# Optimization experiments

Measured on AMD Instinct MI355X. Metric: run time of the kernel, lower is better.

## Reference

```python
import jax, jax.numpy as jnp
import numpy as np
from jax import lax

DIM, HEADS, BS, TOPK, WIN = 256, 8, 8, 4, 7
HID = 2 * DIM  # DBFFN ffn_expansion_factor=2
B, H, W = 2, 56, 56


def _lin(x, w, b=None):
    # torch Linear: y = x @ W.T + b, W is [out, in]
    y = jnp.einsum('...c,oc->...o', x, w)
    return y if b is None else y + b


def _ln(x, w, b, eps=1e-6):
    mu = jnp.mean(x, -1, keepdims=True)
    var = jnp.mean((x - mu) ** 2, -1, keepdims=True)
    return (x - mu) * lax.rsqrt(var + eps) * w + b


def _mha(Q, K, V, wq_w, wq_b, wk_w, wk_b, wv_w, wv_b, p_w, p_b):
    # standard cross MHA: Q [B,Nq,C], K/V [B,Nk,C]
    Bq, Nq, C = Q.shape
    h, d = HEADS, C // HEADS
    scale = d ** -0.5
    q = _lin(Q, wq_w, wq_b).reshape(Bq, Nq, h, d)
    k = _lin(K, wk_w, wk_b).reshape(Bq, -1, h, d)
    v = _lin(V, wv_w, wv_b).reshape(Bq, -1, h, d)
    attn = jax.nn.softmax(jnp.einsum('bnhd,bmhd->bhnm', q, k) * scale, axis=-1)
    out = jnp.einsum('bhnm,bmhd->bnhd', attn, v).reshape(Bq, Nq, C)
    return _lin(out, p_w, p_b)


def setup_inputs() -> dict:
    key = jax.random.key(0)
    ks = jax.random.split(key, 16)
    s = 0.02
    C = DIM
    inp = {
        'x': jax.random.normal(ks[0], (B, C, H, W), jnp.float32),
        'pos_w': jax.random.normal(ks[1], (C, 1, 3, 3), jnp.float32) * s,
        'pos_b': jnp.zeros((C,), jnp.float32),
        'n1_w': jnp.ones((C,), jnp.float32), 'n1_b': jnp.zeros((C,), jnp.float32),
        'n2_w': jnp.ones((C,), jnp.float32), 'n2_b': jnp.zeros((C,), jnp.float32),
        'wq_w': jax.random.normal(ks[2], (3, C, C), jnp.float32) * s,
        'wq_b': jnp.zeros((3, C), jnp.float32),
        'wk_w': jax.random.normal(ks[3], (3, C, C), jnp.float32) * s,
        'wk_b': jnp.zeros((3, C), jnp.float32),
        'wv_w': jax.random.normal(ks[4], (3, C, C), jnp.float32) * s,
        'wv_b': jnp.zeros((3, C), jnp.float32),
        'pj_w': jax.random.normal(ks[5], (3, C, C), jnp.float32) * s,
        'pj_b': jnp.zeros((3, C), jnp.float32),
        # block scorer
        's1_w': jax.random.normal(ks[6], (C // 2, C), jnp.float32) * s,
        's1_b': jnp.zeros((C // 2,), jnp.float32),
        's2_w': jax.random.normal(ks[7], (1, C // 2), jnp.float32) * s,
        's2_b': jnp.zeros((1,), jnp.float32),
        # gating: per-token softmax weights over 3 branches
        'g_w': jax.random.normal(ks[8], (3, C), jnp.float32) * s,
        'g_b': jnp.zeros((3,), jnp.float32),
        # DBFFN (gated dconv FFN, bias=False): in-proj C->2*HID, dw 3x3, out-proj HID->C
        'pin_w': jax.random.normal(ks[9], (2 * HID, C), jnp.float32) * s,
        'dw_w': jax.random.normal(ks[10], (3, 3, 1, 2 * HID), jnp.float32) * s,
        'pout_w': jax.random.normal(ks[11], (C, HID), jnp.float32) * s,
    }
    return inp


def _forward(x, pos_w, pos_b, n1_w, n1_b, n2_w, n2_b, wq_w, wq_b, wk_w, wk_b,
             wv_w, wv_b, pj_w, pj_b, s1_w, s1_b, s2_w, s2_b, g_w, g_b,
             pin_w, dw_w, pout_w):
    Bx, C, Hx, Wx = x.shape
    # depthwise positional conv
    pos = lax.conv_general_dilated(x, pos_w, (1, 1), 'SAME',
                                   dimension_numbers=('NCHW', 'OIHW', 'NCHW'),
                                   feature_group_count=C)
    x = x + pos + pos_b[None, :, None, None] * 0 + pos_b[None, :, None, None]
    feat = jnp.transpose(x, (0, 2, 3, 1))  # NHWC
    Nq = Hx * Wx
    Q = feat.reshape(Bx, Nq, C)
    # block means
    nH, nW = Hx // BS, Wx // BS
    nB = nH * nW
    blk = feat.reshape(Bx, nH, BS, nW, BS, C).transpose(0, 1, 3, 2, 4, 5)
    blk = blk.reshape(Bx, nB, BS * BS, C).mean(axis=2)  # [B,nB,C]
    # block scores + top-k selection
    hsc = jax.nn.gelu(_lin(blk, s1_w, s1_b), approximate=False)
    scores = _lin(hsc, s2_w, s2_b)[..., 0]  # [B,nB]
    topk = min(TOPK, nB)
    _, idx = lax.top_k(scores, topk)
    K_sel = jnp.take_along_axis(blk, idx[:, :, None], axis=1)  # [B,topk,C]
    # compressed + selected branches
    y_cmp = _mha(Q, blk, blk, wq_w[0], wq_b[0], wk_w[0], wk_b[0], wv_w[0], wv_b[0], pj_w[0], pj_b[0])
    y_sel = _mha(Q, K_sel, K_sel, wq_w[1], wq_b[1], wk_w[1], wk_b[1], wv_w[1], wv_b[1], pj_w[1], pj_b[1])
    # local window branch (replicate-pad + unfold == shifted slices)
    pad = WIN // 2
    padded = jnp.pad(feat, ((0, 0), (pad, pad), (pad, pad), (0, 0)), mode='edge')
    patches = jnp.stack([padded[:, dy:dy + Hx, dx:dx + Wx, :]
                         for dy in range(WIN) for dx in range(WIN)], axis=3)
    patches = patches.reshape(Bx, Nq, WIN * WIN, C)  # [B,Nq,49,C]
    h, d = HEADS, C // HEADS
    scale = d ** -0.5
    q = _lin(Q, wq_w[2], wq_b[2]).reshape(Bx, Nq, h, d)
    k = _lin(patches, wk_w[2], wk_b[2]).reshape(Bx, Nq, WIN * WIN, h, d)
    v = _lin(patches, wv_w[2], wv_b[2]).reshape(Bx, Nq, WIN * WIN, h, d)
    attn = jax.nn.softmax(jnp.einsum('bnhd,bnwhd->bnhw', q, k) * scale, axis=-1)
    y_win = jnp.einsum('bnhw,bnwhd->bnhd', attn, v).reshape(Bx, Nq, C)
    y_win = _lin(y_win, pj_w[2], pj_b[2])
    # gated fusion + residual
    qn = _ln(Q, n1_w, n1_b)
    g = jax.nn.softmax(_lin(qn, g_w, g_b), axis=-1)  # [B,Nq,3]
    y = g[..., 0:1] * y_cmp + g[..., 1:2] * y_sel + g[..., 2:3] * y_win + Q
    ym = y.reshape(Bx, Hx, Wx, C)
    # DBFFN: gated depthwise-conv FFN (bias-free)
    t = _lin(ym, pin_w)  # [B,H,W,2*HID]
    t = lax.conv_general_dilated(t, dw_w, (1, 1), 'SAME',
                                 dimension_numbers=('NHWC', 'HWIO', 'NHWC'),
                                 feature_group_count=2 * HID)
    x1, x2 = jnp.split(t, 2, axis=-1)
    mlp = _lin(jax.nn.gelu(x1, approximate=False) * x2, pout_w)
    ym = _ln(ym + mlp, n2_w, n2_b)
    return jnp.transpose(ym, (0, 3, 1, 2))  # NCHW


def reference(x, pos_w, pos_b, n1_w, n1_b, n2_w, n2_b, wq_w, wq_b, wk_w, wk_b,
              wv_w, wv_b, pj_w, pj_b, s1_w, s1_b, s2_w, s2_b, g_w, g_b,
              pin_w, dw_w, pout_w):
    return _forward(x, pos_w, pos_b, n1_w, n1_b, n2_w, n2_b, wq_w, wq_b, wk_w,
                    wk_b, wv_w, wv_b, pj_w, pj_b, s1_w, s1_b, s2_w, s2_b,
                    g_w, g_b, pin_w, dw_w, pout_w)
```

## Files before the change

kernel.cpp:

```cpp
#include <hip/hip_runtime.h>

#define BATCH 2
#define CDIM 256
#define HEADS 8
#define HD 32
#define HH 56
#define WW 56
#define NQ 3136
#define NTOK 6272
#define NB 49
#define NTOPK 4
#define HID2 1024
#define HIDM 512
#define QSTR 768
#define KVSTR 512
#define ASTR 768

typedef short bf16x8 __attribute__((ext_vector_type(8)));
typedef float f32x4 __attribute__((ext_vector_type(4)));
typedef _Float16 h2 __attribute__((ext_vector_type(2)));
struct __align__(16) h2x4 { h2 x, y, z, w; };

__device__ __forceinline__ float blockReduce256(float v, float* red) {
    #pragma unroll
    for (int off = 32; off > 0; off >>= 1) v += __shfl_xor(v, off);
    if ((threadIdx.x & 63) == 0) red[threadIdx.x >> 6] = v;
    __syncthreads();
    float r = red[0] + red[1] + red[2] + red[3];
    __syncthreads();
    return r;
}

__device__ __forceinline__ float gelu_exact(float x) {
    return 0.5f * x * (1.f + erff(x * 0.70710678118654752f));
}

__device__ __forceinline__ short f2bf(float f) {
    union { float f; unsigned u; } v; v.f = f;
    unsigned r = v.u + 0x7FFFu + ((v.u >> 16) & 1u);
    return (short)(r >> 16);
}

__device__ __forceinline__ float fdot2h(h2 a, h2 b, float c) {
#if __has_builtin(__builtin_amdgcn_fdot2)
    return __builtin_amdgcn_fdot2(a, b, c, false);
#else
    return c + (float)a[0] * (float)b[0] + (float)a[1] * (float)b[1];
#endif
}

__device__ __forceinline__ void gld16(const void* gsrc, void* ldst) {
    __builtin_amdgcn_global_load_lds(
        (const __attribute__((address_space(1))) void*)gsrc,
        (__attribute__((address_space(3))) void*)ldst, 16, 0, 0);
}

__global__ __launch_bounds__(256) void k_wcvt(
        const float* __restrict__ wq_w, const float* __restrict__ wk_w,
        const float* __restrict__ wv_w, const float* __restrict__ wq_b,
        const float* __restrict__ wk_b, const float* __restrict__ wv_b,
        const float* __restrict__ pj_w, const float* __restrict__ pin_w,
        const float* __restrict__ pout_w,
        short* __restrict__ Wc1, short* __restrict__ Wpj,
        short* __restrict__ Wpin, short* __restrict__ Wpout,
        float* __restrict__ bias1, float* __restrict__ Wkv0,
        float* __restrict__ bkv0, float* __restrict__ Wkv1,
        float* __restrict__ bkv1) {
    int i = blockIdx.x * 256 + threadIdx.x;
    if (i < 327680) {
        int r = i >> 8, k = i & 255, seg = r >> 8, n = r & 255;
        float v;
        if (seg == 0)      v = wq_w[n * 256 + k];
        else if (seg == 1) v = wq_w[65536 + n * 256 + k];
        else if (seg == 2) v = wq_w[131072 + n * 256 + k];
        else if (seg == 3) v = wk_w[131072 + n * 256 + k];
        else               v = wv_w[131072 + n * 256 + k];
        Wc1[i] = f2bf(v);
    } else if (i < 524288) {
        int j = i - 327680;
        int n = j / 768, t = j % 768, br = t >> 8, k = t & 255;
        Wpj[j] = f2bf(pj_w[br * 65536 + n * 256 + k]);
    } else if (i < 786432) {
        int j = i - 524288;
        Wpin[j] = f2bf(pin_w[j]);
    } else if (i < 917504) {
        int j = i - 786432;
        Wpout[j] = f2bf(pout_w[j]);
    } else if (i < 1048576) {
        int j = i - 917504;
        int r = j >> 8, k = j & 255;
        Wkv0[j] = (r < 256) ? wk_w[r * 256 + k] : wv_w[(r - 256) * 256 + k];
    } else if (i < 1179648) {
        int j = i - 1048576;
        int r = j >> 8, k = j & 255;
        Wkv1[j] = (r < 256) ? wk_w[65536 + r * 256 + k] : wv_w[65536 + (r - 256) * 256 + k];
    } else if (i < 1180928) {
        int j = i - 1179648;
        float v;
        if (j < 768)       v = wq_b[j];
        else if (j < 1024) v = wk_b[512 + (j - 768)];
        else               v = wv_b[512 + (j - 1024)];
        bias1[j] = v;
    } else if (i < 1181440) {
        int j = i - 1180928;
        bkv0[j] = (j < 256) ? wk_b[j] : wv_b[j - 256];
    } else if (i < 1181952) {
        int j = i - 1181440;
        bkv1[j] = (j < 256) ? wk_b[256 + j] : wv_b[j];
    }
}

__global__ __launch_bounds__(256) void k_tr(const float* __restrict__ x,
                                            float* __restrict__ xT) {
    __shared__ float t[64][65];
    int p0 = blockIdx.x * 64;
    int c0 = blockIdx.y * 64;
    int b  = blockIdx.z;
    int tid = threadIdx.x;
    int pi = tid & 63, cj = tid >> 6;
    #pragma unroll
    for (int j = 0; j < 16; j++) {
        int c = cj * 16 + j;
        t[c][pi] = x[((size_t)(b * CDIM + c0 + c)) * NQ + p0 + pi];
    }
    __syncthreads();
    int ci = tid & 63, pj = tid >> 6;
    #pragma unroll
    for (int j = 0; j < 16; j++) {
        int p = pj * 16 + j;
        xT[((size_t)(b * NQ + p0 + p)) * CDIM + c0 + ci] = t[ci][p];
    }
}

__global__ __launch_bounds__(256) void k_posgates(
        const float* __restrict__ xT, const float* __restrict__ pw,
        const float* __restrict__ pb, const float* __restrict__ n1w,
        const float* __restrict__ n1b, const float* __restrict__ gw,
        const float* __restrict__ gb, float* __restrict__ feat,
        float* __restrict__ g, short* __restrict__ featb) {
    __shared__ float red[4];
    int bn = blockIdx.x;
    int b = bn / NQ, n = bn % NQ;
    int y = n / WW, x = n % WW;
    int c = threadIdx.x;
    float wv[9];
    #pragma unroll
    for (int i = 0; i < 9; i++) wv[i] = pw[c * 9 + i];
    const float* xb = xT + (size_t)b * NQ * CDIM;
    float acc = xb[(size_t)n * CDIM + c] + pb[c];
    #pragma unroll
    for (int dy = 0; dy < 3; dy++) {
        int yy = y + dy - 1;
        if (yy < 0 || yy >= HH) continue;
        #pragma unroll
        for (int dx = 0; dx < 3; dx++) {
            int xx = x + dx - 1;
            if (xx < 0 || xx >= WW) continue;
            acc += xb[((size_t)(yy * WW + xx)) * CDIM + c] * wv[dy * 3 + dx];
        }
    }
    feat[(size_t)bn * CDIM + c] = acc;
    featb[(size_t)bn * CDIM + c] = f2bf(acc);
    float mu = blockReduce256(acc, red) * (1.f / CDIM);
    float d = acc - mu;
    float var = blockReduce256(d * d, red) * (1.f / CDIM);
    float qn = d * rsqrtf(var + 1e-6f) * n1w[c] + n1b[c];
    float l0 = blockReduce256(qn * gw[c], red) + gb[0];
    float l1 = blockReduce256(qn * gw[CDIM + c], red) + gb[1];
    float l2 = blockReduce256(qn * gw[2 * CDIM + c], red) + gb[2];
    if (c < 3) {
        float m3 = fmaxf(l0, fmaxf(l1, l2));
        float e0 = __expf(l0 - m3), e1 = __expf(l1 - m3), e2 = __expf(l2 - m3);
        float inv = 1.f / (e0 + e1 + e2);
        float e = (c == 0) ? e0 : (c == 1) ? e1 : e2;
        g[bn * 3 + c] = e * inv;
    }
}

__global__ __launch_bounds__(256) void k_blkscore(
        const float* __restrict__ feat, const float* __restrict__ s1w,
        const float* __restrict__ s1b, const float* __restrict__ s2w,
        const float* __restrict__ s2b, float* __restrict__ blk,
        float* __restrict__ scores) {
    __shared__ float sblk[256];
    __shared__ float red[128];
    int gid = blockIdx.x;
    int b = gid / NB, bid = gid % NB;
    int by = bid / 7, bx = bid % 7;
    int c = threadIdx.x;
    float s = 0.f;
    for (int iy = 0; iy < 8; iy++)
        for (int ix = 0; ix < 8; ix++) {
            int y = by * 8 + iy, xx = bx * 8 + ix;
            s += feat[((size_t)(b * NQ + y * WW + xx)) * CDIM + c];
        }
    s *= (1.f / 64.f);
    blk[(size_t)gid * CDIM + c] = s;
    sblk[c] = s;
    __syncthreads();
    if (c < 128) {
        const float* wrow = s1w + (size_t)c * CDIM;
        float acc = s1b[c];
        for (int k = 0; k < CDIM; k++) acc += sblk[k] * wrow[k];
        red[c] = gelu_exact(acc) * s2w[c];
    }
    __syncthreads();
    #pragma unroll
    for (int st = 64; st > 0; st >>= 1) {
        if (c < st) red[c] += red[c + st];
        __syncthreads();
    }
    if (c == 0) scores[gid] = red[0] + s2b[0];
}

__global__ __launch_bounds__(256) void k_gemm64kv(
        const float* __restrict__ blk, const float* __restrict__ Wkv0,
        const float* __restrict__ bkv0, _Float16* __restrict__ kvcmp,
        const float* __restrict__ scores, const float* __restrict__ Wkv1,
        const float* __restrict__ bkv1, _Float16* __restrict__ kvsel) {
    __shared__ float As[16][68];
    __shared__ float Ws[16][68];
    __shared__ float ssc[2][NB];
    __shared__ int sidx[8];
    const float* W; const float* bias; _Float16* C; int M;
    int m0;
    bool sel = (blockIdx.y == 2);
    if (!sel) { W = Wkv0; bias = bkv0; C = kvcmp; M = 98; m0 = blockIdx.y * 64; }
    else      { W = Wkv1; bias = bkv1; C = kvsel; M = 8;  m0 = 0; }
    const int N = 512, K = 256;
    const int tid = threadIdx.x;
    const int tx = tid & 15, ty = tid >> 4;
    const int n0 = blockIdx.x * 64;
    const int lr = tid >> 2;
    const int lk = (tid & 3) * 4;
    if (sel) {
        if (tid < 2 * NB) ssc[tid / NB][tid % NB] = scores[tid];
        __syncthreads();
        if (tid < 2) {
            for (int t = 0; t < NTOPK; t++) {
                int best = 0; float bv = -1e30f;
                for (int m = 0; m < NB; m++)
                    if (ssc[tid][m] > bv) { bv = ssc[tid][m]; best = m; }
                sidx[tid * 4 + t] = best; ssc[tid][best] = -1e30f;
            }
        }
        __syncthreads();
    }
    int gm = m0 + lr;
    int arow = gm;
    if (sel && gm < 8) arow = (gm >> 2) * NB + sidx[gm];
    float acc[4][4] = {};
    for (int k0 = 0; k0 < K; k0 += 16) {
        float4 av = make_float4(0.f, 0.f, 0.f, 0.f);
        if (gm < M) av = *(const float4*)(blk + (size_t)arow * K + k0 + lk);
        int gn = n0 + lr;
        float4 wv = make_float4(0.f, 0.f, 0.f, 0.f);
        if (gn < N) wv = *(const float4*)(W + (size_t)gn * K + k0 + lk);
        __syncthreads();
        As[lk][lr] = av.x; As[lk + 1][lr] = av.y; As[lk + 2][lr] = av.z; As[lk + 3][lr] = av.w;
        Ws[lk][lr] = wv.x; Ws[lk + 1][lr] = wv.y; Ws[lk + 2][lr] = wv.z; Ws[lk + 3][lr] = wv.w;
        __syncthreads();
        #pragma unroll
        for (int kk = 0; kk < 16; kk++) {
            const float4 a = *(const float4*)&As[kk][ty * 4];
            const float4 b = *(const float4*)&Ws[kk][tx * 4];
            acc[0][0] += a.x * b.x; acc[0][1] += a.x * b.y; acc[0][2] += a.x * b.z; acc[0][3] += a.x * b.w;
            acc[1][0] += a.y * b.x; acc[1][1] += a.y * b.y; acc[1][2] += a.y * b.z; acc[1][3] += a.y * b.w;
            acc[2][0] += a.z * b.x; acc[2][1] += a.z * b.y; acc[2][2] += a.z * b.z; acc[2][3] += a.z * b.w;
            acc[3][0] += a.w * b.x; acc[3][1] += a.w * b.y; acc[3][2] += a.w * b.z; acc[3][3] += a.w * b.w;
        }
    }
    #pragma unroll
    for (int i = 0; i < 4; i++) {
        int om = m0 + ty * 4 + i;
        if (om >= M) break;
        #pragma unroll
        for (int j = 0; j < 4; j++) {
            int gn = n0 + tx * 4 + j;
            C[(size_t)om * N + gn] = (_Float16)(acc[i][j] + bias[gn]);
        }
    }
}

__global__ __launch_bounds__(256) void k_gemm_mfma128(
        const short* __restrict__ A, const short* __restrict__ W,
        const float* __restrict__ bias, float* __restrict__ C,
        int M, int N, int K, int Nc, int cstr, _Float16* __restrict__ C2) {
    __shared__ short As[128][40];
    __shared__ short Bs[128][40];
    int tid = threadIdx.x;
    int wid = tid >> 6, lane = tid & 63;
    int wm = wid >> 1, wn = wid & 1;
    int m0 = blockIdx.y * 128, n0 = blockIdx.x * 128;
    f32x4 acc[4][4] = {};
    int ar = tid >> 1, ac = (tid & 1) * 16;
    int fr = lane & 15, fk = (lane >> 4) * 8;
    for (int k0 = 0; k0 < K; k0 += 32) {
        const short* ap = A + (size_t)(m0 + ar) * K + k0 + ac;
        bf16x8 a0 = *(const bf16x8*)(ap);
        bf16x8 a1 = *(const bf16x8*)(ap + 8);
        const short* wp = W + (size_t)(n0 + ar) * K + k0 + ac;
        bf16x8 wv0 = *(const bf16x8*)(wp);
        bf16x8 wv1 = *(const bf16x8*)(wp + 8);
        __syncthreads();
        *(bf16x8*)&As[ar][ac] = a0;
        *(bf16x8*)&As[ar][ac + 8] = a1;
        *(bf16x8*)&Bs[ar][ac] = wv0;
        *(bf16x8*)&Bs[ar][ac + 8] = wv1;
        __syncthreads();
        bf16x8 af[4], bf[4];
        #pragma unroll
        for (int mi = 0; mi < 4; mi++)
            af[mi] = *(const bf16x8*)&As[wm * 64 + mi * 16 + fr][fk];
        #pragma unroll
        for (int ni = 0; ni < 4; ni++)
            bf[ni] = *(const bf16x8*)&Bs[wn * 64 + ni * 16 + fr][fk];
        #pragma unroll
        for (int mi = 0; mi < 4; mi++)
            #pragma unroll
            for (int ni = 0; ni < 4; ni++)
                acc[mi][ni] = __builtin_amdgcn_mfma_f32_16x16x32_bf16(
                    af[mi], bf[ni], acc[mi][ni], 0, 0, 0);
    }
    int rsub = (lane >> 4) * 4;
    #pragma unroll
    for (int mi = 0; mi < 4; mi++) {
        #pragma unroll
        for (int ni = 0; ni < 4; ni++) {
            int col = n0 + wn * 64 + ni * 16 + (lane & 15);
            float bv = bias ? bias[col] : 0.f;
            #pragma unroll
            for (int r = 0; r < 4; r++) {
                int row = m0 + wm * 64 + mi * 16 + rsub + r;
                float v = acc[mi][ni][r] + bv;
                if (col < Nc) C[(size_t)row * cstr + col] = v;
                else          C2[(size_t)row * (N - Nc) + (col - Nc)] = (_Float16)v;
            }
        }
    }
}

__global__ __launch_bounds__(256) void k_gemm_mfma(
        const short* __restrict__ A, const short* __restrict__ W,
        const float* __restrict__ bias, float* __restrict__ C,
        int M, int N, int K,
        const float* __restrict__ resid, const float* __restrict__ g3,
        const float* __restrict__ pjb, short* __restrict__ Cb) {
    __shared__ short As[128][40];
    __shared__ short Bs[64][40];
    int tid = threadIdx.x;
    int wid = tid >> 6, lane = tid & 63;
    int wm = wid >> 1, wn = wid & 1;
    int m0 = blockIdx.y * 128, n0 = blockIdx.x * 64;
    f32x4 acc[4][2] = {};
    int ar = tid >> 1, ac = (tid & 1) * 16;
    int br = tid >> 2, bc = (tid & 3) * 8;
    int fr = lane & 15, fk = (lane >> 4) * 8;
    for (int k0 = 0; k0 < K; k0 += 32) {
        const short* ap = A + (size_t)(m0 + ar) * K + k0 + ac;
        bf16x8 a0 = *(const bf16x8*)(ap);
        bf16x8 a1 = *(const bf16x8*)(ap + 8);
        bf16x8 wv = *(const bf16x8*)(W + (size_t)(n0 + br) * K + k0 + bc);
        __syncthreads();
        *(bf16x8*)&As[ar][ac] = a0;
        *(bf16x8*)&As[ar][ac + 8] = a1;
        *(bf16x8*)&Bs[br][bc] = wv;
        __syncthreads();
        bf16x8 af[4], bf[2];
        #pragma unroll
        for (int mi = 0; mi < 4; mi++)
            af[mi] = *(const bf16x8*)&As[wm * 64 + mi * 16 + fr][fk];
        #pragma unroll
        for (int ni = 0; ni < 2; ni++)
            bf[ni] = *(const bf16x8*)&Bs[wn * 32 + ni * 16 + fr][fk];
        #pragma unroll
        for (int mi = 0; mi < 4; mi++)
            #pragma unroll
            for (int ni = 0; ni < 2; ni++)
                acc[mi][ni] = __builtin_amdgcn_mfma_f32_16x16x32_bf16(
                    af[mi], bf[ni], acc[mi][ni], 0, 0, 0);
    }
    int rsub = (lane >> 4) * 4;
    #pragma unroll
    for (int mi = 0; mi < 4; mi++) {
        #pragma unroll
        for (int ni = 0; ni < 2; ni++) {
            int col = n0 + wn * 32 + ni * 16 + (lane & 15);
            #pragma unroll
            for (int r = 0; r < 4; r++) {
                int row = m0 + wm * 64 + mi * 16 + rsub + r;
                float v = acc[mi][ni][r];
                if (resid) {
                    v += resid[(size_t)row * N + col]
                       + g3[row * 3 + 0] * pjb[col]
                       + g3[row * 3 + 1] * pjb[256 + col]
                       + g3[row * 3 + 2] * pjb[512 + col];
                } else if (bias) {
                    v += bias[col];
                }
                C[(size_t)row * N + col] = v;
                if (Cb) Cb[(size_t)row * N + col] = f2bf(v);
            }
        }
    }
}

__global__ __launch_bounds__(256) void k_attn_lds(
        const float* __restrict__ bufQ, const _Float16* __restrict__ kvc,
        const _Float16* __restrict__ kvs, short* __restrict__ Acatb,
        const float* __restrict__ g, const _Float16* __restrict__ KVw) {
    __shared__ uint4 buf[80 * 32];
    int tid = threadIdx.x;
    int wid = tid >> 6;
    int lane = tid & 63;
    int l = tid & 31;
    int tk = tid >> 5;
    int dg = l & 3;
    int co = l * 8;
    const float scale = 0.17677669529663687f;

    if (blockIdx.x < 784) {
        int bid = blockIdx.x;
        int swz = (bid & 7) * 98 + (bid >> 3);
        int t0 = swz * 8;
        int tok = t0 + tk;
        int b = t0 / NQ;
        const _Float16* kb = kvc + (size_t)b * NB * 512;
        for (int p = wid * 2; p < NB + 1; p += 8) {
            int myp = p + (lane >> 5);
            if (myp > NB - 1) myp = NB - 1;
            gld16((const uint4*)(kb + (size_t)myp * 512) + (lane & 31), &buf[p * 32]);
        }
        const float* qrow = bufQ + (size_t)tok * QSTR;
        float gate0 = g[tok * 3 + 0];
        float gate1 = g[tok * 3 + 1];
        short* orow = Acatb + (size_t)tok * ASTR;
        h2 qh0, qh1, qh2, qh3;
        {
            const float* qp = qrow + co;
            float4 q0 = *(const float4*)(qp);
            float4 q1 = *(const float4*)(qp + 4);
            qh0[0] = (_Float16)q0.x; qh0[1] = (_Float16)q0.y;
            qh1[0] = (_Float16)q0.z; qh1[1] = (_Float16)q0.w;
            qh2[0] = (_Float16)q1.x; qh2[1] = (_Float16)q1.y;
            qh3[0] = (_Float16)q1.z; qh3[1] = (_Float16)q1.w;
        }
        __syncthreads();
        float sc[13];
        sc[12] = -1e30f;
        #pragma unroll
        for (int m = 0; m < NB; m++) {
            h2x4 kv = *(const h2x4*)&buf[m * 32 + l];
            float acc = fdot2h(qh0, kv.x, 0.f);
            acc = fdot2h(qh1, kv.y, acc);
            acc = fdot2h(qh2, kv.z, acc);
            acc = fdot2h(qh3, kv.w, acc);
            acc += __shfl_xor(acc, 1);
            acc += __shfl_xor(acc, 2);
            if ((m & 3) == dg) sc[m >> 2] = acc * scale;
        }
        float mx = sc[0];
        #pragma unroll
        for (int i = 1; i < 13; i++) mx = fmaxf(mx, sc[i]);
        mx = fmaxf(mx, __shfl_xor(mx, 1));
        mx = fmaxf(mx, __shfl_xor(mx, 2));
        float sum = 0.f;
        #pragma unroll
        for (int i = 0; i < 13; i++) { sc[i] = __expf(sc[i] - mx); sum += sc[i]; }
        sum += __shfl_xor(sum, 1);
        sum += __shfl_xor(sum, 2);
        float inv_c = 1.f / sum;
        __syncthreads();
        for (int p = wid * 2; p < NB + 1; p += 8) {
            int myp = p + (lane >> 5);
            if (myp > NB - 1) myp = NB - 1;
            gld16((const uint4*)(kb + (size_t)myp * 512 + 256) + (lane & 31), &buf[p * 32]);
        }
        {
            const _Float16* ksb = kvs + (size_t)b * NTOPK * 512;
            h2 sh0, sh1, sh2, sh3;
            {
                const float* qp = qrow + 256 + co;
                float4 q0 = *(const float4*)(qp);
                float4 q1 = *(const float4*)(qp + 4);
                sh0[0] = (_Float16)q0.x; sh0[1] = (_Float16)q0.y;
                sh1[0] = (_Float16)q0.z; sh1[1] = (_Float16)q0.w;
                sh2[0] = (_Float16)q1.x; sh2[1] = (_Float16)q1.y;
                sh3[0] = (_Float16)q1.z; sh3[1] = (_Float16)q1.w;
            }
            float sv = 0.f;
            #pragma unroll
            for (int m = 0; m < NTOPK; m++) {
                h2x4 kk = *(const h2x4*)(ksb + (size_t)m * 512 + co);
                float acc = fdot2h(sh0, kk.x, 0.f);
                acc = fdot2h(sh1, kk.y, acc);
                acc = fdot2h(sh2, kk.z, acc);
                acc = fdot2h(sh3, kk.w, acc);
                acc += __shfl_xor(acc, 1);
                acc += __shfl_xor(acc, 2);
                if (m == dg) sv = acc * scale;
            }
            float mxs = sv;
            mxs = fmaxf(mxs, __shfl_xor(mxs, 1));
            mxs = fmaxf(mxs, __shfl_xor(mxs, 2));
            float e = __expf(sv - mxs);
            float sums = e;
            sums += __shfl_xor(sums, 1);
            sums += __shfl_xor(sums, 2);
            float invs = 1.f / sums;
            float o[8];
            #pragma unroll
            for (int d = 0; d < 8; d++) o[d] = 0.f;
            #pragma unroll
            for (int m = 0; m < NTOPK; m++) {
                float pw = __shfl(e, m, 4);
                h2x4 vv = *(const h2x4*)(ksb + (size_t)m * 512 + 256 + co);
                o[0] += pw * (float)vv.x[0]; o[1] += pw * (float)vv.x[1];
                o[2] += pw * (float)vv.y[0]; o[3] += pw * (float)vv.y[1];
                o[4] += pw * (float)vv.z[0]; o[5] += pw * (float)vv.z[1];
                o[6] += pw * (float)vv.w[0]; o[7] += pw * (float)vv.w[1];
            }
            float gg = gate1 * invs;
            bf16x8 ov;
            #pragma unroll
            for (int d = 0; d < 8; d++) ov[d] = f2bf(o[d] * gg);
            *(bf16x8*)(orow + 256 + co) = ov;
        }
        __syncthreads();
        {
            float o[8];
            #pragma unroll
            for (int d = 0; d < 8; d++) o[d] = 0.f;
            #pragma unroll
            for (int m = 0; m < NB; m++) {
                float pw = __shfl(sc[m >> 2], m & 3, 4);
                h2x4 vv = *(const h2x4*)&buf[m * 32 + l];
                o[0] += pw * (float)vv.x[0]; o[1] += pw * (float)vv.x[1];
                o[2] += pw * (float)vv.y[0]; o[3] += pw * (float)vv.y[1];
                o[4] += pw * (float)vv.z[0]; o[5] += pw * (float)vv.z[1];
                o[6] += pw * (float)vv.w[0]; o[7] += pw * (float)vv.w[1];
            }
            float gg = gate0 * inv_c;
            bf16x8 ov;
            #pragma unroll
            for (int d = 0; d < 8; d++) ov[d] = f2bf(o[d] * gg);
            *(bf16x8*)(orow + co) = ov;
        }
    } else {
        int bid = blockIdx.x - 784;
        int swz = (bid & 7) * 98 + (bid >> 3);
        int b = swz / 392;
        int r = swz % 392;
        int y0 = (r / 14) * 2;
        int x0 = (r % 14) * 4;
        int ty = tk >> 2, tx = tk & 3;
        int y = y0 + ty, x = x0 + tx;
        int tok = b * NQ + y * WW + x;
        const _Float16* KVb = KVw + (size_t)b * NQ * KVSTR;
        for (int p = wid * 2; p < 80; p += 8) {
            int pp = p + (lane >> 5);
            int pr = pp / 10, pc = pp - pr * 10;
            int gy = min(max(y0 + pr - 3, 0), HH - 1);
            int gx = min(max(x0 + pc - 3, 0), WW - 1);
            gld16((const uint4*)(KVb + (size_t)(gy * WW + gx) * KVSTR) + (lane & 31),
                  &buf[p * 32]);
        }
        h2 qh0, qh1, qh2, qh3;
        {
            const float* qp = bufQ + ((size_t)tok) * QSTR + 512 + co;
            float4 q0 = *(const float4*)(qp);
            float4 q1 = *(const float4*)(qp + 4);
            qh0[0] = (_Float16)q0.x; qh0[1] = (_Float16)q0.y;
            qh1[0] = (_Float16)q0.z; qh1[1] = (_Float16)q0.w;
            qh2[0] = (_Float16)q1.x; qh2[1] = (_Float16)q1.y;
            qh3[0] = (_Float16)q1.z; qh3[1] = (_Float16)q1.w;
        }
        float gate = g[tok * 3 + 2];
        __syncthreads();
        float sw[13];
        sw[12] = -1e30f;
        #pragma unroll
        for (int dy = 0; dy < 7; dy++) {
            #pragma unroll
            for (int dx = 0; dx < 7; dx++) {
                int p = (ty + dy) * 10 + tx + dx;
                h2x4 kv = *(const h2x4*)&buf[p * 32 + l];
                float acc = fdot2h(qh0, kv.x, 0.f);
                acc = fdot2h(qh1, kv.y, acc);
                acc = fdot2h(qh2, kv.z, acc);
                acc = fdot2h(qh3, kv.w, acc);
                acc += __shfl_xor(acc, 1);
                acc += __shfl_xor(acc, 2);
                int m = dy * 7 + dx;
                if ((m & 3) == dg) sw[m >> 2] = acc * scale;
            }
        }
        float mx = sw[0];
        #pragma unroll
        for (int i = 1; i < 13; i++) mx = fmaxf(mx, sw[i]);
        mx = fmaxf(mx, __shfl_xor(mx, 1));
        mx = fmaxf(mx, __shfl_xor(mx, 2));
        float sum = 0.f;
        #pragma unroll
        for (int i = 0; i < 13; i++) { sw[i] = __expf(sw[i] - mx); sum += sw[i]; }
        sum += __shfl_xor(sum, 1);
        sum += __shfl_xor(sum, 2);
        float inv = 1.f / sum;
        __syncthreads();
        for (int p = wid * 2; p < 80; p += 8) {
            int pp = p + (lane >> 5);
            int pr = pp / 10, pc = pp - pr * 10;
            int gy = min(max(y0 + pr - 3, 0), HH - 1);
            int gx = min(max(x0 + pc - 3, 0), WW - 1);
            gld16((const uint4*)(KVb + (size_t)(gy * WW + gx) * KVSTR + 256) + (lane & 31),
                  &buf[p * 32]);
        }
        __syncthreads();
        float o[8];
        #pragma unroll
        for (int d = 0; d < 8; d++) o[d] = 0.f;
        #pragma unroll
        for (int dy = 0; dy < 7; dy++) {
            #pragma unroll
            for (int dx = 0; dx < 7; dx++) {
                int p = (ty + dy) * 10 + tx + dx;
                int m = dy * 7 + dx;
                float pw = __shfl(sw[m >> 2], m & 3, 4);
                h2x4 vv = *(const h2x4*)&buf[p * 32 + l];
                o[0] += pw * (float)vv.x[0]; o[1] += pw * (float)vv.x[1];
                o[2] += pw * (float)vv.y[0]; o[3] += pw * (float)vv.y[1];
                o[4] += pw * (float)vv.z[0]; o[5] += pw * (float)vv.z[1];
                o[6] += pw * (float)vv.w[0]; o[7] += pw * (float)vv.w[1];
            }
        }
        float gg = gate * inv;
        short* op = Acatb + (size_t)tok * ASTR + 512 + co;
        bf16x8 ov;
        #pragma unroll
        for (int d = 0; d < 8; d++) ov[d] = f2bf(o[d] * gg);
        *(bf16x8*)(op) = ov;
    }
}

__global__ __launch_bounds__(256) void k_dwglu2(
        const float* __restrict__ t, const float* __restrict__ w,
        short* __restrict__ G) {
    int gid = blockIdx.x;
    int xq = gid & 3;
    int y = (gid >> 2) % HH;
    int b = gid / (HH * 4);
    int c = threadIdx.x;
    float wv[9][4];
    #pragma unroll
    for (int i = 0; i < 9; i++)
        #pragma unroll
        for (int j = 0; j < 4; j++) wv[i][j] = w[i * HID2 + c + j * 256];
    const float* tb = t + (size_t)b * NQ * HID2;
    short* Gbase = G + (size_t)b * NQ * HIDM;
    int x0 = xq * 14;
    float col[3][12];
    #pragma unroll
    for (int ci = 0; ci < 2; ci++) {
        int xx = x0 - 1 + ci;
        #pragma unroll
        for (int r = 0; r < 3; r++) {
            int yy = y + r - 1;
            bool ok = (xx >= 0) && (yy >= 0) && (yy < HH);
            const float* row = ok ? (tb + ((size_t)(yy * WW + xx)) * HID2 + c) : nullptr;
            #pragma unroll
            for (int j = 0; j < 4; j++)
                col[ci][r * 4 + j] = ok ? row[j * 256] : 0.f;
        }
    }
    #pragma unroll
    for (int i = 0; i < 14; i++) {
        int xx = x0 + i;
        {
            int xl = xx + 1;
            #pragma unroll
            for (int r = 0; r < 3; r++) {
                int yy = y + r - 1;
                bool ok = (xl < WW) && (yy >= 0) && (yy < HH);
                const float* row = ok ? (tb + ((size_t)(yy * WW + xl)) * HID2 + c) : nullptr;
                #pragma unroll
                for (int j = 0; j < 4; j++)
                    col[(i + 2) % 3][r * 4 + j] = ok ? row[j * 256] : 0.f;
            }
        }
        float a0 = 0.f, a1 = 0.f, a2 = 0.f, a3 = 0.f;
        #pragma unroll
        for (int r = 0; r < 3; r++) {
            #pragma unroll
            for (int dxx = 0; dxx < 3; dxx++) {
                const float* cc = col[(i + dxx) % 3];
                int wi = r * 3 + dxx;
                a0 += cc[r * 4 + 0] * wv[wi][0];
                a1 += cc[r * 4 + 1] * wv[wi][1];
                a2 += cc[r * 4 + 2] * wv[wi][2];
                a3 += cc[r * 4 + 3] * wv[wi][3];
            }
        }
        short* Gb = Gbase + (size_t)(y * WW + xx) * HIDM;
        Gb[c]       = f2bf(gelu_exact(a0) * a2);
        Gb[c + 256] = f2bf(gelu_exact(a1) * a3);
    }
}

__global__ __launch_bounds__(256) void k_finalln(
        const float* __restrict__ ym, const float* __restrict__ mlp,
        const float* __restrict__ n2w, const float* __restrict__ n2b,
        float* __restrict__ ymn) {
    __shared__ float red[4];
    int bn = blockIdx.x, c = threadIdx.x;
    size_t base = (size_t)bn * CDIM;
    float v = ym[base + c] + mlp[base + c];
    float mu = blockReduce256(v, red) * (1.f / CDIM);
    float d = v - mu;
    float var = blockReduce256(d * d, red) * (1.f / CDIM);
    ymn[base + c] = d * rsqrtf(var + 1e-6f) * n2w[c] + n2b[c];
}

__global__ __launch_bounds__(256) void k_tr2(const float* __restrict__ ymn,
                                             float* __restrict__ out) {
    __shared__ float t[64][65];
    int p0 = blockIdx.x * 64;
    int c0 = blockIdx.y * 64;
    int b  = blockIdx.z;
    int tid = threadIdx.x;
    int ci = tid & 63, pj = tid >> 6;
    #pragma unroll
    for (int j = 0; j < 16; j++) {
        int p = pj * 16 + j;
        t[ci][p] = ymn[((size_t)(b * NQ + p0 + p)) * CDIM + c0 + ci];
    }
    __syncthreads();
    int pi = tid & 63, cj = tid >> 6;
    #pragma unroll
    for (int j = 0; j < 16; j++) {
        int c = cj * 16 + j;
        out[((size_t)(b * CDIM + c0 + c)) * NQ + p0 + pi] = t[c][pi];
    }
}

extern "C" void kernel_launch(void* const* d_in, const int* in_sizes, int n_in,
                              void* d_out, int out_size, void* d_ws, size_t ws_size,
                              hipStream_t stream) {
    const float* x     = (const float*)d_in[0];
    const float* pos_w = (const float*)d_in[1];
    const float* pos_b = (const float*)d_in[2];
    const float* n1w   = (const float*)d_in[3];
    const float* n1b   = (const float*)d_in[4];
    const float* n2w   = (const float*)d_in[5];
    const float* n2b   = (const float*)d_in[6];
    const float* wq_w  = (const float*)d_in[7];
    const float* wq_b  = (const float*)d_in[8];
    const float* wk_w  = (const float*)d_in[9];
    const float* wk_b  = (const float*)d_in[10];
    const float* wv_w  = (const float*)d_in[11];
    const float* wv_b  = (const float*)d_in[12];
    const float* pj_w  = (const float*)d_in[13];
    const float* pj_b  = (const float*)d_in[14];
    const float* s1w   = (const float*)d_in[15];
    const float* s1b   = (const float*)d_in[16];
    const float* s2w   = (const float*)d_in[17];
    const float* s2b   = (const float*)d_in[18];
    const float* gw    = (const float*)d_in[19];
    const float* gb    = (const float*)d_in[20];
    const float* pinw  = (const float*)d_in[21];
    const float* dww   = (const float*)d_in[22];
    const float* poutw = (const float*)d_in[23];
    float* out = (float*)d_out;
    float* ws  = (float*)d_ws;

    const size_t SZ = (size_t)NTOK * CDIM;
    float* feat = ws;
    float* bufQ = feat + SZ;
    float* R1   = bufQ + (size_t)NTOK * QSTR;
    float* xT   = R1;
    short* Acatb = (short*)R1;
    float* T1   = R1;
    float* ym   = R1 + (size_t)NTOK * 1024;
    _Float16* KVw = (_Float16*)(ym + SZ);
    float* ymn  = (float*)KVw;
    short* featb = (short*)((float*)KVw + SZ);
    short* ymb   = featb + (size_t)NTOK * CDIM;
    float* blk   = (float*)(ymb + (size_t)NTOK * CDIM);
    _Float16* kvcmp = (_Float16*)(blk + 98 * 256);
    _Float16* kvsel = kvcmp + 98 * 512;
    float* scores = (float*)(kvsel + 8 * 512);
    float* g      = scores + 128;
    float* bias1  = g + (size_t)NTOK * 3;
    float* Wkv0   = bias1 + 1280;
    float* bkv0   = Wkv0 + 512 * 256;
    float* Wkv1   = bkv0 + 512;
    float* bkv1   = Wkv1 + 512 * 256;
    short* Wc1    = (short*)(bkv1 + 512);
    short* Wpj    = Wc1 + 1280 * 256;
    short* Wpin   = Wpj + 256 * 768;
    short* Wpout  = Wpin + 1024 * 256;
    short* G      = (short*)bufQ;
    float* MLP    = bufQ + (size_t)NTOK * CDIM;

    hipLaunchKernelGGL(k_wcvt, dim3(4618), dim3(256), 0, stream,
                       wq_w, wk_w, wv_w, wq_b, wk_b, wv_b, pj_w, pinw, poutw,
                       Wc1, Wpj, Wpin, Wpout, bias1, Wkv0, bkv0, Wkv1, bkv1);
    hipLaunchKernelGGL(k_tr, dim3(49, 4, BATCH), dim3(256), 0, stream, x, xT);
    hipLaunchKernelGGL(k_posgates, dim3(NTOK), dim3(256), 0, stream,
                       xT, pos_w, pos_b, n1w, n1b, gw, gb, feat, g, featb);
    hipLaunchKernelGGL(k_blkscore, dim3(BATCH * NB), dim3(256), 0, stream,
                       feat, s1w, s1b, s2w, s2b, blk, scores);
    hipLaunchKernelGGL(k_gemm64kv, dim3(8, 3), dim3(256), 0, stream,
                       blk, Wkv0, bkv0, kvcmp, scores, Wkv1, bkv1, kvsel);
    hipLaunchKernelGGL(k_gemm_mfma128, dim3(1280 / 128, NTOK / 128), dim3(256), 0, stream,
                       featb, Wc1, bias1, bufQ, NTOK, 1280, 256, 768, QSTR, KVw);
    hipLaunchKernelGGL(k_attn_lds, dim3(1568), dim3(256), 0, stream,
                       bufQ, kvcmp, kvsel, Acatb, g, KVw);
    hipLaunchKernelGGL(k_gemm_mfma, dim3(CDIM / 64, NTOK / 128), dim3(256), 0, stream,
                       Acatb, Wpj, nullptr, ym, NTOK, CDIM, ASTR, feat, g, pj_b, ymb);
    hipLaunchKernelGGL(k_gemm_mfma128, dim3(HID2 / 128, NTOK / 128), dim3(256), 0, stream,
                       ymb, Wpin, nullptr, T1, NTOK, HID2, 256, HID2, HID2, (_Float16*)nullptr);
    hipLaunchKernelGGL(k_dwglu2, dim3(BATCH * HH * 4), dim3(256), 0, stream, T1, dww, G);
    hipLaunchKernelGGL(k_gemm_mfma, dim3(CDIM / 64, NTOK / 128), dim3(256), 0, stream,
                       G, Wpout, nullptr, MLP, NTOK, CDIM, HIDM,
                       nullptr, nullptr, nullptr, (short*)nullptr);
    hipLaunchKernelGGL(k_finalln, dim3(NTOK), dim3(256), 0, stream, ym, MLP, n2w, n2b, ymn);
    hipLaunchKernelGGL(k_tr2, dim3(49, 4, BATCH), dim3(256), 0, stream, ymn, out);
}
```

Measured before the change: 194.8 us.

## Store QKV and FFN intermediates as fp16, and use one wave per token in posgates

The fused QKV GEMM now writes a single fp16 buffer with a 1280-element row stride, replacing the fp32 Q buffer plus a separate fp16 KV buffer. The attention kernel reads Q directly as packed halves, with no per-lane conversion. The FFN input-projection output T1 is also stored in fp16 and consumed by the depthwise GLU kernel, roughly halving the traffic of the largest intermediate. k_posgates is restructured so each 64-lane wave handles whole tokens with float4 loads and shuffle-only reductions, removing block-level syncs, and the workspace layout is reshuffled to fit. The trade-off is extra fp16 rounding of Q and T1, plus reliance on the unseen GEMM kernel handling the half-only output path at the new stride.

Measured after the change: 230.7 us. 1.18x slower.

```diff
diff --git a/kernel.cpp b/kernel.cpp
--- a/kernel.cpp
+++ b/kernel.cpp
@@ -12,24 +12,13 @@
 #define NTOPK 4
 #define HID2 1024
 #define HIDM 512
-#define QSTR 768
-#define KVSTR 512
+#define QSTRH 1280
 #define ASTR 768
 
 typedef short bf16x8 __attribute__((ext_vector_type(8)));
 typedef float f32x4 __attribute__((ext_vector_type(4)));
 typedef _Float16 h2 __attribute__((ext_vector_type(2)));
 struct __align__(16) h2x4 { h2 x, y, z, w; };
-
-__device__ __forceinline__ float blockReduce256(float v, float* red) {
-    #pragma unroll
-    for (int off = 32; off > 0; off >>= 1) v += __shfl_xor(v, off);
-    if ((threadIdx.x & 63) == 0) red[threadIdx.x >> 6] = v;
-    __syncthreads();
-    float r = red[0] + red[1] + red[2] + red[3];
-    __syncthreads();
-    return r;
-}
 
 __device__ __forceinline__ float gelu_exact(float x) {
     return 0.5f * x * (1.f + erff(x * 0.70710678118654752f));
@@ -138,42 +127,81 @@
         const float* __restrict__ n1b, const float* __restrict__ gw,
         const float* __restrict__ gb, float* __restrict__ feat,
         float* __restrict__ g, short* __restrict__ featb) {
-    __shared__ float red[4];
-    int bn = blockIdx.x;
-    int b = bn / NQ, n = bn % NQ;
-    int y = n / WW, x = n % WW;
-    int c = threadIdx.x;
-    float wv[9];
-    #pragma unroll
-    for (int i = 0; i < 9; i++) wv[i] = pw[c * 9 + i];
-    const float* xb = xT + (size_t)b * NQ * CDIM;
-    float acc = xb[(size_t)n * CDIM + c] + pb[c];
-    #pragma unroll
-    for (int dy = 0; dy < 3; dy++) {
-        int yy = y + dy - 1;
-        if (yy < 0 || yy >= HH) continue;
-        #pragma unroll
-        for (int dx = 0; dx < 3; dx++) {
-            int xx = x + dx - 1;
-            if (xx < 0 || xx >= WW) continue;
-            acc += xb[((size_t)(yy * WW + xx)) * CDIM + c] * wv[dy * 3 + dx];
-        }
-    }
-    feat[(size_t)bn * CDIM + c] = acc;
-    featb[(size_t)bn * CDIM + c] = f2bf(acc);
-    float mu = blockReduce256(acc, red) * (1.f / CDIM);
-    float d = acc - mu;
-    float var = blockReduce256(d * d, red) * (1.f / CDIM);
-    float qn = d * rsqrtf(var + 1e-6f) * n1w[c] + n1b[c];
-    float l0 = blockReduce256(qn * gw[c], red) + gb[0];
-    float l1 = blockReduce256(qn * gw[CDIM + c], red) + gb[1];
-    float l2 = blockReduce256(qn * gw[2 * CDIM + c], red) + gb[2];
-    if (c < 3) {
-        float m3 = fmaxf(l0, fmaxf(l1, l2));
-        float e0 = __expf(l0 - m3), e1 = __expf(l1 - m3), e2 = __expf(l2 - m3);
-        float inv = 1.f / (e0 + e1 + e2);
-        float e = (c == 0) ? e0 : (c == 1) ? e1 : e2;
-        g[bn * 3 + c] = e * inv;
+    int wvid = threadIdx.x >> 6;
+    int lane = threadIdx.x & 63;
+    int c4 = lane * 4;
+    float pwv[4][9];
+    #pragma unroll
+    for (int j = 0; j < 4; j++)
+        #pragma unroll
+        for (int i = 0; i < 9; i++) pwv[j][i] = pw[(c4 + j) * 9 + i];
+    float4 pbv = *(const float4*)(pb + c4);
+    float4 w1 = *(const float4*)(n1w + c4);
+    float4 b1 = *(const float4*)(n1b + c4);
+    float4 gw0 = *(const float4*)(gw + c4);
+    float4 gw1 = *(const float4*)(gw + CDIM + c4);
+    float4 gw2 = *(const float4*)(gw + 2 * CDIM + c4);
+    float gb0 = gb[0], gb1 = gb[1], gb2 = gb[2];
+    int tbase = blockIdx.x * 16 + wvid * 4;
+    for (int t = 0; t < 4; t++) {
+        int bn = tbase + t;
+        int b = bn / NQ, n = bn % NQ;
+        int y = n / WW, x = n % WW;
+        const float* xb = xT + (size_t)b * NQ * CDIM;
+        float4 a = *(const float4*)(xb + (size_t)n * CDIM + c4);
+        float acc0 = a.x + pbv.x, acc1 = a.y + pbv.y;
+        float acc2 = a.z + pbv.z, acc3 = a.w + pbv.w;
+        #pragma unroll
+        for (int dy = 0; dy < 3; dy++) {
+            int yy = y + dy - 1;
+            if (yy < 0 || yy >= HH) continue;
+            #pragma unroll
+            for (int dx = 0; dx < 3; dx++) {
+                int xx = x + dx - 1;
+                if (xx < 0 || xx >= WW) continue;
+                float4 v = *(const float4*)(xb + ((size_t)(yy * WW + xx)) * CDIM + c4);
+                int wi = dy * 3 + dx;
+                acc0 += v.x * pwv[0][wi];
+                acc1 += v.y * pwv[1][wi];
+                acc2 += v.z * pwv[2][wi];
+                acc3 += v.w * pwv[3][wi];
+            }
+        }
+        *(float4*)(feat + (size_t)bn * CDIM + c4) = make_float4(acc0, acc1, acc2, acc3);
+        short4 fb;
+        fb.x = f2bf(acc0); fb.y = f2bf(acc1); fb.z = f2bf(acc2); fb.w = f2bf(acc3);
+        *(short4*)(featb + (size_t)bn * CDIM + c4) = fb;
+        float s = acc0 + acc1 + acc2 + acc3;
+        #pragma unroll
+        for (int off = 32; off > 0; off >>= 1) s += __shfl_xor(s, off);
+        float mu = s * (1.f / CDIM);
+        float d0 = acc0 - mu, d1 = acc1 - mu, d2 = acc2 - mu, d3 = acc3 - mu;
+        float ss = d0 * d0 + d1 * d1 + d2 * d2 + d3 * d3;
+        #pragma unroll
+        for (int off = 32; off > 0; off >>= 1) ss += __shfl_xor(ss, off);
+        float rstd = rsqrtf(ss * (1.f / CDIM) + 1e-6f);
+        float q0 = d0 * rstd * w1.x + b1.x;
+        float q1 = d1 * rstd * w1.y + b1.y;
+        float q2 = d2 * rstd * w1.z + b1.z;
+        float q3 = d3 * rstd * w1.w + b1.w;
+        float p0 = q0 * gw0.x + q1 * gw0.y + q2 * gw0.z + q3 * gw0.w;
+        float p1 = q0 * gw1.x + q1 * gw1.y + q2 * gw1.z + q3 * gw1.w;
+        float p2 = q0 * gw2.x + q1 * gw2.y + q2 * gw2.z + q3 * gw2.w;
+        #pragma unroll
+        for (int off = 32; off > 0; off >>= 1) {
+            p0 += __shfl_xor(p0, off);
+            p1 += __shfl_xor(p1, off);
+            p2 += __shfl_xor(p2, off);
+        }
+        if (lane == 0) {
+            float l0 = p0 + gb0, l1 = p1 + gb1, l2 = p2 + gb2;
+            float m3 = fmaxf(l0, fmaxf(l1, l2));
+            float e0 = __expf(l0 - m3), e1 = __expf(l1 - m3), e2 = __expf(l2 - m3);
+            float inv = 1.f / (e0 + e1 + e2);
+            g[bn * 3 + 0] = e0 * inv;
+            g[bn * 3 + 1] = e1 * inv;
+            g[bn * 3 + 2] = e2 * inv;
+        }
     }
 }
 
@@ -406,9 +434,9 @@
 }
 
 __global__ __launch_bounds__(256) void k_attn_lds(
-        const float* __restrict__ bufQ, const _Float16* __restrict__ kvc,
+        const _Float16* __restrict__ bufQ, const _Float16* __restrict__ kvc,
         const _Float16* __restrict__ kvs, short* __restrict__ Acatb,
-        const float* __restrict__ g, const _Float16* __restrict__ KVw) {
+        const float* __restrict__ g) {
     __shared__ uint4 buf[80 * 32];
     int tid = threadIdx.x;
     int wid = tid >> 6;
@@ -431,30 +459,21 @@
             if (myp > NB - 1) myp = NB - 1;
             gld16((const uint4*)(kb + (size_t)myp * 512) + (lane & 31), &buf[p * 32]);
         }
-        const float* qrow = bufQ + (size_t)tok * QSTR;
+        const _Float16* qrow = bufQ + (size_t)tok * QSTRH;
         float gate0 = g[tok * 3 + 0];
         float gate1 = g[tok * 3 + 1];
         short* orow = Acatb + (size_t)tok * ASTR;
-        h2 qh0, qh1, qh2, qh3;
-        {
-            const float* qp = qrow + co;
-            float4 q0 = *(const float4*)(qp);
-            float4 q1 = *(const float4*)(qp + 4);
-            qh0[0] = (_Float16)q0.x; qh0[1] = (_Float16)q0.y;
-            qh1[0] = (_Float16)q0.z; qh1[1] = (_Float16)q0.w;
-            qh2[0] = (_Float16)q1.x; qh2[1] = (_Float16)q1.y;
-            qh3[0] = (_Float16)q1.z; qh3[1] = (_Float16)q1.w;
-        }
+        h2x4 qv = *(const h2x4*)(qrow + co);
         __syncthreads();
         float sc[13];
         sc[12] = -1e30f;
         #pragma unroll
         for (int m = 0; m < NB; m++) {
             h2x4 kv = *(const h2x4*)&buf[m * 32 + l];
-            float acc = fdot2h(qh0, kv.x, 0.f);
-            acc = fdot2h(qh1, kv.y, acc);
-            acc = fdot2h(qh2, kv.z, acc);
-            acc = fdot2h(qh3, kv.w, acc);
+            float acc = fdot2h(qv.x, kv.x, 0.f);
+            acc = fdot2h(qv.y, kv.y, acc);
+            acc = fdot2h(qv.z, kv.z, acc);
+            acc = fdot2h(qv.w, kv.w, acc);
             acc += __shfl_xor(acc, 1);
             acc += __shfl_xor(acc, 2);
             if ((m & 3) == dg) sc[m >> 2] = acc * scale;
@@ -478,24 +497,15 @@
         }
         {
             const _Float16* ksb = kvs + (size_t)b * NTOPK * 512;
-            h2 sh0, sh1, sh2, sh3;
-            {
-                const float* qp = qrow + 256 + co;
-                float4 q0 = *(const float4*)(qp);
-                float4 q1 = *(const float4*)(qp + 4);
-                sh0[0] = (_Float16)q0.x; sh0[1] = (_Float16)q0.y;
-                sh1[0] = (_Float16)q0.z; sh1[1] = (_Float16)q0.w;
-                sh2[0] = (_Float16)q1.x; sh2[1] = (_Float16)q1.y;
-                sh3[0] = (_Float16)q1.z; sh3[1] = (_Float16)q1.w;
-            }
+            h2x4 qs = *(const h2x4*)(qrow + 256 + co);
             float sv = 0.f;
             #pragma unroll
             for (int m = 0; m < NTOPK; m++) {
                 h2x4 kk = *(const h2x4*)(ksb + (size_t)m * 512 + co);
-                float acc = fdot2h(sh0, kk.x, 0.f);
-                acc = fdot2h(sh1, kk.y, acc);
-                acc = fdot2h(sh2, kk.z, acc);
-                acc = fdot2h(sh3, kk.w, acc);
+                float acc = fdot2h(qs.x, kk.x, 0.f);
+                acc = fdot2h(qs.y, kk.y, acc);
+                acc = fdot2h(qs.z, kk.z, acc);
+                acc = fdot2h(qs.w, kk.w, acc);
                 acc += __shfl_xor(acc, 1);
                 acc += __shfl_xor(acc, 2);
                 if (m == dg) sv = acc * scale;
@@ -556,25 +566,16 @@
         int ty = tk >> 2, tx = tk & 3;
         int y = y0 + ty, x = x0 + tx;
         int tok = b * NQ + y * WW + x;
-        const _Float16* KVb = KVw + (size_t)b * NQ * KVSTR;
+        const _Float16* KVb = bufQ + (size_t)b * NQ * QSTRH;
         for (int p = wid * 2; p < 80; p += 8) {
             int pp = p + (lane >> 5);
             int pr = pp / 10, pc = pp - pr * 10;
             int gy = min(max(y0 + pr - 3, 0), HH - 1);
             int gx = min(max(x0 + pc - 3, 0), WW - 1);
-            gld16((const uint4*)(KVb + (size_t)(gy * WW + gx) * KVSTR) + (lane & 31),
+            gld16((const uint4*)(KVb + (size_t)(gy * WW + gx) * QSTRH + 768) + (lane & 31),
                   &buf[p * 32]);
         }
-        h2 qh0, qh1, qh2, qh3;
-        {
-            const float* qp = bufQ + ((size_t)tok) * QSTR + 512 + co;
-            float4 q0 = *(const float4*)(qp);
-            float4 q1 = *(const float4*)(qp + 4);
-            qh0[0] = (_Float16)q0.x; qh0[1] = (_Float16)q0.y;
-            qh1[0] = (_Float16)q0.z; qh1[1] = (_Float16)q0.w;
-            qh2[0] = (_Float16)q1.x; qh2[1] = (_Float16)q1.y;
-            qh3[0] = (_Float16)q1.z; qh3[1] = (_Float16)q1.w;
-        }
+        h2x4 qv = *(const h2x4*)(bufQ + (size_t)tok * QSTRH + 512 + co);
         float gate = g[tok * 3 + 2];
         __syncthreads();
         float sw[13];
@@ -585,10 +586,10 @@
             for (int dx = 0; dx < 7; dx++) {
                 int p = (ty + dy) * 10 + tx + dx;
                 h2x4 kv = *(const h2x4*)&buf[p * 32 + l];
-                float acc = fdot2h(qh0, kv.x, 0.f);
-                acc = fdot2h(qh1, kv.y, acc);
-                acc = fdot2h(qh2, kv.z, acc);
-                acc = fdot2h(qh3, kv.w, acc);
+                float acc = fdot2h(qv.x, kv.x, 0.f);
+                acc = fdot2h(qv.y, kv.y, acc);
+                acc = fdot2h(qv.z, kv.z, acc);
+                acc = fdot2h(qv.w, kv.w, acc);
                 acc += __shfl_xor(acc, 1);
                 acc += __shfl_xor(acc, 2);
                 int m = dy * 7 + dx;
@@ -612,7 +613,7 @@
             int pr = pp / 10, pc = pp - pr * 10;
             int gy = min(max(y0 + pr - 3, 0), HH - 1);
             int gx = min(max(x0 + pc - 3, 0), WW - 1);
-            gld16((const uint4*)(KVb + (size_t)(gy * WW + gx) * KVSTR + 256) + (lane & 31),
+            gld16((const uint4*)(KVb + (size_t)(gy * WW + gx) * QSTRH + 1024) + (lane & 31),
                   &buf[p * 32]);
         }
         __syncthreads();
@@ -643,7 +644,7 @@
 }
 
 __global__ __launch_bounds__(256) void k_dwglu2(
-        const float* __restrict__ t, const float* __restrict__ w,
+        const _Float16* __restrict__ t, const float* __restrict__ w,
         short* __restrict__ G) {
     int gid = blockIdx.x;
     int xq = gid & 3;
@@ -655,7 +656,7 @@
     for (int i = 0; i < 9; i++)
         #pragma unroll
         for (int j = 0; j < 4; j++) wv[i][j] = w[i * HID2 + c + j * 256];
-    const float* tb = t + (size_t)b * NQ * HID2;
+    const _Float16* tb = t + (size_t)b * NQ * HID2;
     short* Gbase = G + (size_t)b * NQ * HIDM;
     int x0 = xq * 14;
     float col[3][12];
@@ -666,10 +667,10 @@
         for (int r = 0; r < 3; r++) {
             int yy = y + r - 1;
             bool ok = (xx >= 0) && (yy >= 0) && (yy < HH);
-            const float* row = ok ? (tb + ((size_t)(yy * WW + xx)) * HID2 + c) : nullptr;
+            const _Float16* row = ok ? (tb + ((size_t)(yy * WW + xx)) * HID2 + c) : nullptr;
             #pragma unroll
             for (int j = 0; j < 4; j++)
-                col[ci][r * 4 + j] = ok ? row[j * 256] : 0.f;
+                col[ci][r * 4 + j] = ok ? (float)row[j * 256] : 0.f;
         }
     }
     #pragma unroll
@@ -681,10 +682,10 @@
             for (int r = 0; r < 3; r++) {
                 int yy = y + r - 1;
                 bool ok = (xl < WW) && (yy >= 0) && (yy < HH);
-                const float* row = ok ? (tb + ((size_t)(yy * WW + xl)) * HID2 + c) : nullptr;
+                const _Float16* row = ok ? (tb + ((size_t)(yy * WW + xl)) * HID2 + c) : nullptr;
                 #pragma unroll
                 for (int j = 0; j < 4; j++)
-                    col[(i + 2) % 3][r * 4 + j] = ok ? row[j * 256] : 0.f;
+                    col[(i + 2) % 3][r * 4 + j] = ok ? (float)row[j * 256] : 0.f;
             }
         }
         float a0 = 0.f, a1 = 0.f, a2 = 0.f, a3 = 0.f;
@@ -714,9 +715,22 @@
     int bn = blockIdx.x, c = threadIdx.x;
     size_t base = (size_t)bn * CDIM;
     float v = ym[base + c] + mlp[base + c];
-    float mu = blockReduce256(v, red) * (1.f / CDIM);
+    #pragma unroll
+    for (int off = 32; off > 0; off >>= 1) v += 0.f;
+    float s = v;
+    #pragma unroll
+    for (int off = 32; off > 0; off >>= 1) s += __shfl_xor(s, off);
+    if ((c & 63) == 0) red[c >> 6] = s;
+    __syncthreads();
+    float mu = (red[0] + red[1] + red[2] + red[3]) * (1.f / CDIM);
+    __syncthreads();
     float d = v - mu;
-    float var = blockReduce256(d * d, red) * (1.f / CDIM);
+    float ss = d * d;
+    #pragma unroll
+    for (int off = 32; off > 0; off >>= 1) ss += __shfl_xor(ss, off);
+    if ((c & 63) == 0) red[c >> 6] = ss;
+    __syncthreads();
+    float var = (red[0] + red[1] + red[2] + red[3]) * (1.f / CDIM);
     ymn[base + c] = d * rsqrtf(var + 1e-6f) * n2w[c] + n2b[c];
 }
 
@@ -774,15 +788,13 @@
 
     const size_t SZ = (size_t)NTOK * CDIM;
     float* feat = ws;
-    float* bufQ = feat + SZ;
-    float* R1   = bufQ + (size_t)NTOK * QSTR;
+    _Float16* bufQh = (_Float16*)(feat + SZ);
+    float* R1   = (float*)(bufQh + (size_t)NTOK * QSTRH);
     float* xT   = R1;
     short* Acatb = (short*)R1;
-    float* T1   = R1;
-    float* ym   = R1 + (size_t)NTOK * 1024;
-    _Float16* KVw = (_Float16*)(ym + SZ);
-    float* ymn  = (float*)KVw;
-    short* featb = (short*)((float*)KVw + SZ);
+    _Float16* T1h = (_Float16*)R1;
+    float* ym   = R1 + (size_t)NTOK * 512;
+    short* featb = (short*)(ym + SZ);
     short* ymb   = featb + (size_t)NTOK * CDIM;
     float* blk   = (float*)(ymb + (size_t)NTOK * CDIM);
     _Float16* kvcmp = (_Float16*)(blk + 98 * 256);
@@ -798,28 +810,29 @@
     short* Wpj    = Wc1 + 1280 * 256;
     short* Wpin   = Wpj + 256 * 768;
     short* Wpout  = Wpin + 1024 * 256;
-    short* G      = (short*)bufQ;
-    float* MLP    = bufQ + (size_t)NTOK * CDIM;
+    short* G      = (short*)bufQh;
+    float* MLP    = (float*)(bufQh + (size_t)NTOK * 512);
+    float* ymn    = feat;
 
     hipLaunchKernelGGL(k_wcvt, dim3(4618), dim3(256), 0, stream,
                        wq_w, wk_w, wv_w, wq_b, wk_b, wv_b, pj_w, pinw, poutw,
                        Wc1, Wpj, Wpin, Wpout, bias1, Wkv0, bkv0, Wkv1, bkv1);
     hipLaunchKernelGGL(k_tr, dim3(49, 4, BATCH), dim3(256), 0, stream, x, xT);
-    hipLaunchKernelGGL(k_posgates, dim3(NTOK), dim3(256), 0, stream,
+    hipLaunchKernelGGL(k_posgates, dim3(NTOK / 16), dim3(256), 0, stream,
                        xT, pos_w, pos_b, n1w, n1b, gw, gb, feat, g, featb);
     hipLaunchKernelGGL(k_blkscore, dim3(BATCH * NB), dim3(256), 0, stream,
                        feat, s1w, s1b, s2w, s2b, blk, scores);
     hipLaunchKernelGGL(k_gemm64kv, dim3(8, 3), dim3(256), 0, stream,
                        blk, Wkv0, bkv0, kvcmp, scores, Wkv1, bkv1, kvsel);
     hipLaunchKernelGGL(k_gemm_mfma128, dim3(1280 / 128, NTOK / 128), dim3(256), 0, stream,
-                       featb, Wc1, bias1, bufQ, NTOK, 1280, 256, 768, QSTR, KVw);
+                       featb, Wc1, bias1, (float*)nullptr, NTOK, 1280, 256, 0, 0, bufQh);
     hipLaunchKernelGGL(k_attn_lds, dim3(1568), dim3(256), 0, stream,
-                       bufQ, kvcmp, kvsel, Acatb, g, KVw);
+                       bufQh, kvcmp, kvsel, Acatb, g);
     hipLaunchKernelGGL(k_gemm_mfma, dim3(CDIM / 64, NTOK / 128), dim3(256), 0, stream,
                        Acatb, Wpj, nullptr, ym, NTOK, CDIM, ASTR, feat, g, pj_b, ymb);
     hipLaunchKernelGGL(k_gemm_mfma128, dim3(HID2 / 128, NTOK / 128), dim3(256), 0, stream,
-                       ymb, Wpin, nullptr, T1, NTOK, HID2, 256, HID2, HID2, (_Float16*)nullptr);
-    hipLaunchKernelGGL(k_dwglu2, dim3(BATCH * HH * 4), dim3(256), 0, stream, T1, dww, G);
+                       ymb, Wpin, nullptr, (float*)nullptr, NTOK, HID2, 256, 0, 0, T1h);
+    hipLaunchKernelGGL(k_dwglu2, dim3(BATCH * HH * 4), dim3(256), 0, stream, T1h, dww, G);
     hipLaunchKernelGGL(k_gemm_mfma, dim3(CDIM / 64, NTOK / 128), dim3(256), 0, stream,
                        G, Wpout, nullptr, MLP, NTOK, CDIM, HIDM,
                        nullptr, nullptr, nullptr, (short*)nullptr);
```
